# Kernel tuning notes

Measured on AMD Instinct MI355X. Metric: run time of the kernel, lower is better.

Reference implementation:

```python
import jax, jax.numpy as jnp
import numpy as np
from jax import lax

EPS = 1e-5  # torch BatchNorm default eps

# Binarization with straight-through estimator (hard-tanh gradient window),
# matching BinaryFunc in dizcza/MCMC_BinaryNet.
@jax.custom_vjp
def binarize(x):
    return jnp.sign(x)

def _bin_fwd(x):
    return jnp.sign(x), x

def _bin_bwd(res, g):
    return (g * (jnp.abs(res) <= 1.0).astype(g.dtype),)

binarize.defvjp(_bin_fwd, _bin_bwd)

def bn2d(x, gamma, beta):
    # training-mode BatchNorm2d: batch stats over (N,H,W), biased variance
    m = x.mean(axis=(0, 2, 3), keepdims=True)
    v = x.var(axis=(0, 2, 3), keepdims=True)
    xn = (x - m) * lax.rsqrt(v + EPS)
    return xn * gamma[None, :, None, None] + beta[None, :, None, None]

def bn1d(x, gamma, beta):
    m = x.mean(axis=0, keepdims=True)
    v = x.var(axis=0, keepdims=True)
    return (x - m) * lax.rsqrt(v + EPS) * gamma[None, :] + beta[None, :]

def bconv(x, w):
    # BinaryDecorator(Conv2d): sign(x) conv sign(W), padding=0, no bias
    return lax.conv_general_dilated(binarize(x), binarize(w), (1, 1), 'VALID',
                                    dimension_numbers=('NCHW', 'OIHW', 'NCHW'))

def maxpool2(x):
    return lax.reduce_window(x, -jnp.inf, lax.max, (1, 1, 2, 2), (1, 1, 2, 2), 'VALID')

def prelu(x, a):
    return jnp.where(x >= 0, x, a * x)


def setup_inputs() -> dict:
    key = jax.random.key(0)
    ks = iter(jax.random.split(key, 16))
    conv_channels = [3, 128, 256, 512]
    fc_sizes = [512 * 6 * 6, 1024, 10]
    d = {'x': jax.random.normal(next(ks), (128, 3, 64, 64), jnp.float32)}
    for i, (cin, cout) in enumerate(zip(conv_channels[:-1], conv_channels[1:])):
        d[f'cg{i}'] = jnp.ones((cin,), jnp.float32)          # BN2d gamma
        d[f'cb{i}'] = jnp.zeros((cin,), jnp.float32)         # BN2d beta
        d[f'cw{i}'] = jax.random.normal(next(ks), (cout, cin, 3, 3), jnp.float32) * 0.05
        d[f'cp{i}'] = jnp.full((1,), 0.25, jnp.float32)      # PReLU (num_parameters=1)
    for i, (fin, fout) in enumerate(zip(fc_sizes[:-1], fc_sizes[1:])):
        d[f'fg{i}'] = jnp.ones((fin,), jnp.float32)
        d[f'fb{i}'] = jnp.zeros((fin,), jnp.float32)
        d[f'fw{i}'] = jax.random.normal(next(ks), (fout, fin), jnp.float32) * 0.05
        d[f'fp{i}'] = jnp.full((1,), 0.25, jnp.float32)
    d['scale'] = jnp.full((1,), 1e-3, jnp.float32)           # ScaleLayer init
    return d


def reference(x, cg0, cb0, cw0, cp0, cg1, cb1, cw1, cp1, cg2, cb2, cw2, cp2,
              fg0, fb0, fw0, fp0, fg1, fb1, fw1, fp1, scale):
    for cg, cb, cw, cp in ((cg0, cb0, cw0, cp0), (cg1, cb1, cw1, cp1), (cg2, cb2, cw2, cp2)):
        x = bn2d(x, cg, cb)
        x = bconv(x, cw)
        x = maxpool2(x)
        x = prelu(x, cp)
    x = x.reshape(x.shape[0], -1)  # [B, 512*6*6]
    for fg, fb, fw, fp in ((fg0, fb0, fw0, fp0), (fg1, fb1, fw1, fp1)):
        x = bn1d(x, fg, fb)
        x = binarize(x) @ binarize(fw).T  # BinaryDecorator(Linear), no bias
        x = prelu(x, fp)
    return x * scale
```

## Files before the change

kernel.cpp:

```cpp
#include <hip/hip_runtime.h>
#include <cstdint>
#include <cstddef>

#define BN_EPS 1e-5


__global__ void zero_d(double* p, int n) {
  int i = blockIdx.x * blockDim.x + threadIdx.x;
  if (i < n) p[i] = 0.0;
}

__global__ void reduce_plane_p(const float* __restrict__ x, double* __restrict__ pp,
                               int C, int HW) {
  int c = blockIdx.x, n = blockIdx.y;
  const float* p = x + ((long)n * C + c) * HW;
  double s = 0.0, s2 = 0.0;
  for (int i = threadIdx.x; i < HW; i += blockDim.x) {
    double v = (double)p[i];
    s += v; s2 += v * v;
  }
  for (int o = 32; o > 0; o >>= 1) {
    s  += __shfl_down(s, o, 64);
    s2 += __shfl_down(s2, o, 64);
  }
  __shared__ double ls[4], ls2[4];
  int lane = threadIdx.x & 63, w = threadIdx.x >> 6;
  if (lane == 0) { ls[w] = s; ls2[w] = s2; }
  __syncthreads();
  if (threadIdx.x == 0) {
    double a = 0, b = 0;
    for (int i = 0; i < 4; i++) { a += ls[i]; b += ls2[i]; }
    long o = ((long)n * C + c) * 2;
    pp[o] = a; pp[o + 1] = b;
  }
}

__global__ void finalize_plane_par(const double* __restrict__ pp, double2* __restrict__ st,
                                   int C, int N, double cnt) {
  int c = blockIdx.x;
  double s = 0.0, s2 = 0.0;
  for (int n = threadIdx.x; n < N; n += blockDim.x) {
    long o = ((long)n * C + c) * 2;
    s  += pp[o];
    s2 += pp[o + 1];
  }
  for (int o = 32; o > 0; o >>= 1) {
    s  += __shfl_down(s, o, 64);
    s2 += __shfl_down(s2, o, 64);
  }
  __shared__ double ls[2], ls2[2];
  int lane = threadIdx.x & 63, w = threadIdx.x >> 6;
  if (lane == 0) { ls[w] = s; ls2[w] = s2; }
  __syncthreads();
  if (threadIdx.x == 0) {
    double a = ls[0] + ls[1], b = ls2[0] + ls2[1];
    double m = a / cnt;
    double v = b / cnt - m * m;
    st[c] = make_double2(m, 1.0 / sqrt(v + BN_EPS));
  }
}

__global__ void reduce_cl_p(const float* __restrict__ x, double* __restrict__ part,
                            int C, long rows) {
  int lane = threadIdx.x & 63, wv = threadIdx.x >> 6;
  int c = blockIdx.x * 64 + lane;
  double s = 0.0, s2 = 0.0;
  for (long r = (long)blockIdx.y * 4 + wv; r < rows; r += (long)gridDim.y * 4) {
    double v = (double)x[r * C + c];
    s += v; s2 += v * v;
  }
  __shared__ double ls[4][64], ls2[4][64];
  ls[wv][lane] = s; ls2[wv][lane] = s2;
  __syncthreads();
  if (threadIdx.x < 64) {
    double a = ls[0][lane] + ls[1][lane] + ls[2][lane] + ls[3][lane];
    double b = ls2[0][lane] + ls2[1][lane] + ls2[2][lane] + ls2[3][lane];
    long o = (long)blockIdx.y * 2 * C + 2 * c;
    part[o] = a; part[o + 1] = b;
  }
}

__global__ void finalize_parts_par(const double* __restrict__ part, double2* __restrict__ st,
                                   int C, int Y, double cnt) {
  int c = blockIdx.x;
  double s = 0.0, s2 = 0.0;
  for (int y = threadIdx.x; y < Y; y += blockDim.x) {
    long o = (long)y * 2 * C + 2 * c;
    s  += part[o];
    s2 += part[o + 1];
  }
  for (int o = 32; o > 0; o >>= 1) {
    s  += __shfl_down(s, o, 64);
    s2 += __shfl_down(s2, o, 64);
  }
  __shared__ double ls[4], ls2[4];
  int lane = threadIdx.x & 63, w = threadIdx.x >> 6;
  if (lane == 0) { ls[w] = s; ls2[w] = s2; }
  __syncthreads();
  if (threadIdx.x == 0) {
    double a = ls[0] + ls[1] + ls[2] + ls[3];
    double b = ls2[0] + ls2[1] + ls2[2] + ls2[3];
    double m = a / cnt;
    double v = b / cnt - m * m;
    st[c] = make_double2(m, 1.0 / sqrt(v + BN_EPS));
  }
}

__global__ void reduce_cols2(const float* __restrict__ x, double* __restrict__ sums,
                             int R, int F, int RS) {
  int f = blockIdx.x * blockDim.x + threadIdx.x;
  int r0 = blockIdx.y * RS, r1 = min(r0 + RS, R);
  double s = 0.0, s2 = 0.0;
  for (int r = r0; r < r1; r++) {
    double v = (double)x[(long)r * F + f];
    s += v; s2 += v * v;
  }
  atomicAdd(&sums[2 * f], s);
  atomicAdd(&sums[2 * f + 1], s2);
}

__global__ void finalize_stats(const double* __restrict__ sums, double2* __restrict__ st,
                               int C, double cnt) {
  int c = blockIdx.x * blockDim.x + threadIdx.x;
  if (c >= C) return;
  double m = sums[2 * c] / cnt;
  double v = sums[2 * c + 1] / cnt - m * m;
  st[c] = make_double2(m, 1.0 / sqrt(v + BN_EPS));
}


__global__ void pack_bits_c1(const float* __restrict__ x, const double2* __restrict__ st,
                             const float* __restrict__ g, const float* __restrict__ b,
                             uint64_t* __restrict__ rows, int nwid) {
  long base = ((long)blockIdx.x * 4 + (threadIdx.x >> 6)) * 8;
  int lane = threadIdx.x & 63;
  for (int j = 0; j < 8; j++) {
    long wid = base + j;
    if (wid >= nwid) return;
    int n = (int)(wid / 192), rem = (int)(wid % 192);
    int ci = rem >> 6, y = rem & 63;
    double2 s = st[ci];
    float xv = x[(((long)n * 3 + ci) * 64 + y) * 64 + lane];
    float xn = (float)(((double)xv - s.x) * s.y) * g[ci] + b[ci];
    uint64_t m = __ballot(xn > 0.f);
    if (lane == 0) rows[wid] = m;
  }
}

__global__ void pack_wc1(const float* __restrict__ w, uint32_t* __restrict__ wm) {
  int co = threadIdx.x;
  uint32_t m = 0;
  for (int j = 0; j < 27; j++) m |= (uint32_t)(w[co * 27 + j] > 0.f) << j;
  wm[co] = m;
}

__global__ void pack_cl(const float* __restrict__ acl, const double2* __restrict__ st,
                        const float* __restrict__ g, const float* __restrict__ b,
                        uint64_t* __restrict__ out, int C, long nwords, int lw) {
  long base = ((long)blockIdx.x * 4 + (threadIdx.x >> 6)) * 8;
  int lane = threadIdx.x & 63;
  for (int j = 0; j < 8; j++) {
    long wid = base + j;
    if (wid >= nwords) return;
    long row = wid >> lw;
    int w = (int)(wid & ((1 << lw) - 1));
    int c = w * 64 + lane;
    double2 s = st[c];
    float xv = acl[row * C + c];
    float xn = (float)(((double)xv - s.x) * s.y) * g[c] + b[c];
    uint64_t m = __ballot(xn > 0.f);
    if (lane == 0) out[wid] = m;
  }
}

__global__ void pack_wconv(const float* __restrict__ w, uint64_t* __restrict__ out,
                           int CO, int CI, int W) {
  int i = blockIdx.x * blockDim.x + threadIdx.x;
  int total = CO * 9 * W;
  if (i >= total) return;
  int wd = i % W;
  int t = i / W;
  int tap = t % 9, co = t / 9;
  uint64_t bits = 0;
  for (int k = 0; k < 64; k++) {
    int ci = wd * 64 + k;
    bits |= (uint64_t)(w[((long)co * CI + ci) * 9 + tap] > 0.f) << k;
  }
  out[i] = bits;
}

__global__ void pack_nz(const float* __restrict__ x, const double2* __restrict__ st,
                        const float* __restrict__ g, const float* __restrict__ b,
                        uint64_t* __restrict__ out, int R, int F) {
  int Wf = F >> 6;
  long base = ((long)blockIdx.x * 4 + (threadIdx.x >> 6)) * 8;
  int lane = threadIdx.x & 63;
  for (int j = 0; j < 8; j++) {
    long wid = base + j;
    if (wid >= (long)R * Wf) return;
    long r = wid / Wf;
    int w = (int)(wid % Wf);
    int f = w * 64 + lane;
    double2 s = st[f];
    double d = (double)x[r * F + f] - s.x;
    float xn = (float)(d * s.y) * g[f] + b[f];
    uint64_t sm = __ballot(xn > 0.f);
    uint64_t nm = __ballot(d != 0.0);
    if (lane == 0) { out[2 * wid] = sm; out[2 * wid + 1] = nm; }
  }
}

__global__ void pack_wfc2_t(const float* __restrict__ w, uint64_t* __restrict__ out,
                            int O, int F) {
  int Wf = F >> 6;
  long base = ((long)blockIdx.x * 4 + (threadIdx.x >> 6)) * 8;
  int lane = threadIdx.x & 63;
  for (int j = 0; j < 8; j++) {
    long wid = base + j;
    if (wid >= (long)O * Wf) return;
    long o = wid / Wf;
    int wd = (int)(wid % Wf);
    uint64_t m = __ballot(w[o * F + wd * 64 + lane] > 0.f);
    if (lane == 0) out[(long)wd * O + o] = m;
  }
}


__global__ __launch_bounds__(256) void conv1_pool3(const uint64_t* __restrict__ rows,
                                                   const uint32_t* __restrict__ wm,
                                                   const float* __restrict__ cp,
                                                   float* __restrict__ out) {
  __shared__ uint64_t rL[192];
  __shared__ uint32_t wL[128];
  __shared__ uint32_t mL[61 * 4];
  int n = blockIdx.y, chunk = blockIdx.x, t = threadIdx.x;
  if (t < 192) rL[t] = rows[n * 192 + t];
  if (t < 128) wL[t] = wm[t];
  __syncthreads();
  if (t < 244) {
    int pl = t >> 2, quad = t & 3;
    int pos = chunk * 61 + pl;
    if (pos < 961) {
      int py = pos / 31, px = pos - py * 31;
      int cy = 2 * py + (quad >> 1), cx = 2 * px + (quad & 1);
      uint32_t m = 0;
#pragma unroll
      for (int ci = 0; ci < 3; ci++)
#pragma unroll
        for (int ky = 0; ky < 3; ky++)
          m |= (uint32_t)((rL[ci * 64 + cy + ky] >> cx) & 7) << (ci * 9 + ky * 3);
      mL[pl * 4 + quad] = m;
    }
  }
  __syncthreads();
  int co = t & 127, slot = t >> 7;
  float alpha = cp[0];
  uint32_t w = wL[co];
  for (int i = slot; i < 61; i += 2) {
    int pos = chunk * 61 + i;
    if (pos >= 961) break;
    int p0 = __popc(mL[4 * i] ^ w);
    int p1 = __popc(mL[4 * i + 1] ^ w);
    int p2 = __popc(mL[4 * i + 2] ^ w);
    int p3 = __popc(mL[4 * i + 3] ^ w);
    int dot = 27 - 2 * min(min(p0, p1), min(p2, p3));
    float f = (float)dot;
    out[((long)n * 961 + pos) * 128 + co] = dot >= 0 ? f : alpha * f;
  }
}

template <int W, int IH, int PH, int CHUNK, bool CL>
__global__ __attribute__((amdgpu_flat_work_group_size(256, 256),
                          amdgpu_waves_per_eu(3, 4)))
void convp_carry(const uint64_t* __restrict__ in, const uint64_t* __restrict__ wt,
                 const float* __restrict__ cp, float* __restrict__ out, int CO) {
  __shared__ uint64_t sIn[10 * IH * W];
  int n = blockIdx.y;
  int cg = blockIdx.x / CHUNK, chunk = blockIdx.x % CHUNK;
  int t = threadIdx.x, lane = t & 63, slot = t >> 6;
  int r0 = chunk * 8;
  int nr = min(10, IH - r0);
  const uint64_t* src = in + ((long)n * IH + r0) * (IH * W);
  for (int i = t; i < nr * IH * W; i += 256) sIn[i] = src[i];
  int co = cg * 64 + lane;
  uint64_t wr[9 * W];
  const uint64_t* wg = wt + (long)co * (9 * W);
#pragma unroll
  for (int i = 0; i < 9 * W; i++) wr[i] = wg[i];
  __syncthreads();
  int py = chunk * 4 + slot;
  if (py >= PH) return;
  float alpha = cp[0];
  const int K = 9 * 64 * W;
  const uint64_t* base = &sIn[(2 * slot) * (IH * W)];
  uint64_t c[4][2 * W];
#pragma unroll
  for (int cy = 0; cy < 4; cy++) {
    const uint64_t* p = &base[(cy * IH) * W];
#pragma unroll
    for (int j = 0; j < 2 * W; j++) c[cy][j] = p[j];
  }
#pragma unroll
  for (int px = 0; px < PH; px++) {
    int a00 = 0, a01 = 0, a10 = 0, a11 = 0;
#pragma unroll
    for (int cy = 0; cy < 4; cy++) {
      uint64_t f[2 * W];
      const uint64_t* fp = &base[(cy * IH + 2 * px + 2) * W];
#pragma unroll
      for (int j = 0; j < 2 * W; j++) f[j] = fp[j];
#pragma unroll
      for (int col = 0; col < 4; col++) {
#pragma unroll
        for (int wd = 0; wd < W; wd++) {
          uint64_t v = (col < 2) ? c[cy][col * W + wd] : f[(col - 2) * W + wd];
#pragma unroll
          for (int dy = 0; dy < 2; dy++) {
            int ky = cy - dy;
            if (ky < 0 || ky > 2) continue;
#pragma unroll
            for (int dx = 0; dx < 2; dx++) {
              int kx = col - dx;
              if (kx < 0 || kx > 2) continue;
              int p = __popcll(v ^ wr[(ky * 3 + kx) * W + wd]);
              if (dy == 0) { if (dx == 0) a00 += p; else a01 += p; }
              else         { if (dx == 0) a10 += p; else a11 += p; }
            }
          }
        }
      }
#pragma unroll
      for (int j = 0; j < 2 * W; j++) c[cy][j] = f[j];
    }
    int dot = K - 2 * min(min(a00, a01), min(a10, a11));
    float f = (float)dot;
    long idx = CL ? (((long)n * PH * PH + py * PH + px) * CO + co)
                  : (((long)n * CO + co) * PH * PH + (py * PH + px));
    out[idx] = dot >= 0 ? f : alpha * f;
  }
}

#define TAP2(acc, P, wa, wb) acc += __popcll((P).x ^ (wa)) + __popcll((P).y ^ (wb));
#define ROWT(aL, aR, pA, pB, pC, pD, WX, WY, WZ)                \
  TAP2(aL, pA, WX.x, WX.y) TAP2(aL, pB, WY.x, WY.y)             \
  TAP2(aL, pC, WZ.x, WZ.y)                                      \
  TAP2(aR, pB, WX.x, WX.y) TAP2(aR, pC, WY.x, WY.y)             \
  TAP2(aR, pD, WZ.x, WZ.y)

__global__ __attribute__((amdgpu_flat_work_group_size(256, 256),
                          amdgpu_waves_per_eu(4, 6)))
void convs3(const uint64_t* __restrict__ in, const uint64_t* __restrict__ wt,
            const float* __restrict__ cp, float* __restrict__ out) {
  __shared__ uint64_t sIn[14 * 14 * 4];
  int n = blockIdx.y, cg = blockIdx.x;
  int t = threadIdx.x, lane = t & 63, slot = t >> 6;
  const uint64_t* src = in + (long)n * 784;
  for (int i = t; i < 784; i += 256) sIn[i] = src[i];
  int h = lane >> 5;
  int co = cg * 32 + (lane & 31);
  const uint64_t* wg = wt + co * 36 + 2 * h;
  ulonglong2 W0 = *(const ulonglong2*)(wg + 0);
  ulonglong2 W1 = *(const ulonglong2*)(wg + 4);
  ulonglong2 W2 = *(const ulonglong2*)(wg + 8);
  ulonglong2 W3 = *(const ulonglong2*)(wg + 12);
  ulonglong2 W4 = *(const ulonglong2*)(wg + 16);
  ulonglong2 W5 = *(const ulonglong2*)(wg + 20);
  ulonglong2 W6 = *(const ulonglong2*)(wg + 24);
  ulonglong2 W7 = *(const ulonglong2*)(wg + 28);
  ulonglong2 W8 = *(const ulonglong2*)(wg + 32);
  __syncthreads();
  float alpha = cp[0];
  float* outb = out + ((long)n * 512 + co) * 36;
#pragma unroll
  for (int k = 0; k < 9; k++) {
    int pos = slot + 4 * k;
    int py = pos / 6, px = pos - py * 6;
    const uint64_t* q = sIn + ((2 * py) * 14 + 2 * px) * 4 + 2 * h;
    int a00 = 0, a01 = 0, a10 = 0, a11 = 0;
    {
      ulonglong2 p0 = *(const ulonglong2*)(q + 0);
      ulonglong2 p1 = *(const ulonglong2*)(q + 4);
      ulonglong2 p2 = *(const ulonglong2*)(q + 8);
      ulonglong2 p3 = *(const ulonglong2*)(q + 12);
      ROWT(a00, a01, p0, p1, p2, p3, W0, W1, W2)
    }
    {
      const uint64_t* q1 = q + 56;
      ulonglong2 p0 = *(const ulonglong2*)(q1 + 0);
      ulonglong2 p1 = *(const ulonglong2*)(q1 + 4);
      ulonglong2 p2 = *(const ulonglong2*)(q1 + 8);
      ulonglong2 p3 = *(const ulonglong2*)(q1 + 12);
      ROWT(a00, a01, p0, p1, p2, p3, W3, W4, W5)
      ROWT(a10, a11, p0, p1, p2, p3, W0, W1, W2)
    }
    {
      const uint64_t* q2 = q + 112;
      ulonglong2 p0 = *(const ulonglong2*)(q2 + 0);
      ulonglong2 p1 = *(const ulonglong2*)(q2 + 4);
      ulonglong2 p2 = *(const ulonglong2*)(q2 + 8);
      ulonglong2 p3 = *(const ulonglong2*)(q2 + 12);
      ROWT(a00, a01, p0, p1, p2, p3, W6, W7, W8)
      ROWT(a10, a11, p0, p1, p2, p3, W3, W4, W5)
    }
    {
      const uint64_t* q3 = q + 168;
      ulonglong2 p0 = *(const ulonglong2*)(q3 + 0);
      ulonglong2 p1 = *(const ulonglong2*)(q3 + 4);
      ulonglong2 p2 = *(const ulonglong2*)(q3 + 8);
      ulonglong2 p3 = *(const ulonglong2*)(q3 + 12);
      ROWT(a10, a11, p0, p1, p2, p3, W6, W7, W8)
    }
    int t00 = a00 + __shfl_xor(a00, 32);
    int t01 = a01 + __shfl_xor(a01, 32);
    int t10 = a10 + __shfl_xor(a10, 32);
    int t11 = a11 + __shfl_xor(a11, 32);
    if (h == 0) {
      int dot = 2304 - 2 * min(min(t00, t01), min(t10, t11));
      float ff = (float)dot;
      outb[pos] = dot >= 0 ? ff : alpha * ff;
    }
  }
}


__global__ void fc_bin2(const uint64_t* __restrict__ xp, const uint64_t* __restrict__ wp_t,
                        const float* __restrict__ cp, float* __restrict__ out,
                        int O, int Wf) {
  __shared__ uint64_t xs[2][288], xz[2][288];
  int r0 = blockIdx.y * 2;
  for (int i = threadIdx.x; i < 2 * Wf; i += blockDim.x) {
    int rr = i / Wf, wd = i - rr * Wf;
    xs[rr][wd] = xp[(((long)(r0 + rr)) * Wf + wd) * 2];
    xz[rr][wd] = xp[(((long)(r0 + rr)) * Wf + wd) * 2 + 1];
  }
  __syncthreads();
  int o = blockIdx.x * blockDim.x + threadIdx.x;
  if (o >= O) return;
  int pc0 = 0, pc1 = 0, nz0 = 0, nz1 = 0;
  for (int wd = 0; wd < Wf; wd++) {
    uint64_t w = wp_t[(long)wd * O + o];
    uint64_t z0 = xz[0][wd], z1 = xz[1][wd];
    pc0 += __popcll((xs[0][wd] ^ w) & z0);
    pc1 += __popcll((xs[1][wd] ^ w) & z1);
    nz0 += __popcll(z0);
    nz1 += __popcll(z1);
  }
  float alpha = cp[0];
  int d0 = nz0 - 2 * pc0, d1 = nz1 - 2 * pc1;
  float f0 = (float)d0, f1 = (float)d1;
  out[(long)r0 * O + o] = d0 >= 0 ? f0 : alpha * f0;
  out[(long)(r0 + 1) * O + o] = d1 >= 0 ? f1 : alpha * f1;
}

__global__ void fc_bin_scale(const uint64_t* __restrict__ xp, const uint64_t* __restrict__ wp_t,
                             const float* __restrict__ cp, const float* __restrict__ scale,
                             float* __restrict__ out, int R, int O, int Wf) {
  int i = blockIdx.x * blockDim.x + threadIdx.x;
  if (i >= R * O) return;
  int o = i % O, r = i / O;
  int pc = 0, nzc = 0;
  for (int wd = 0; wd < Wf; wd++) {
    uint64_t nz = xp[((long)r * Wf + wd) * 2 + 1];
    pc += __popcll((xp[((long)r * Wf + wd) * 2] ^ wp_t[(long)wd * O + o]) & nz);
    nzc += __popcll(nz);
  }
  int dot = nzc - 2 * pc;
  float f = (float)dot;
  float alpha = cp[0];
  f = dot >= 0 ? f : alpha * f;
  out[i] = f * scale[0];
}


extern "C" void kernel_launch(void* const* d_in, const int* in_sizes, int n_in,
                              void* d_out, int out_size, void* d_ws, size_t ws_size,
                              hipStream_t stream) {
  const float* x   = (const float*)d_in[0];
  const float* cg0 = (const float*)d_in[1];
  const float* cb0 = (const float*)d_in[2];
  const float* cw0 = (const float*)d_in[3];
  const float* cp0 = (const float*)d_in[4];
  const float* cg1 = (const float*)d_in[5];
  const float* cb1 = (const float*)d_in[6];
  const float* cw1 = (const float*)d_in[7];
  const float* cp1 = (const float*)d_in[8];
  const float* cg2 = (const float*)d_in[9];
  const float* cb2 = (const float*)d_in[10];
  const float* cw2 = (const float*)d_in[11];
  const float* cp2 = (const float*)d_in[12];
  const float* fg0 = (const float*)d_in[13];
  const float* fb0 = (const float*)d_in[14];
  const float* fw0 = (const float*)d_in[15];
  const float* fp0 = (const float*)d_in[16];
  const float* fg1 = (const float*)d_in[17];
  const float* fb1 = (const float*)d_in[18];
  const float* fw1 = (const float*)d_in[19];
  const float* fp1 = (const float*)d_in[20];
  const float* scl = (const float*)d_in[21];

  char* ws = (char*)d_ws;
  size_t off = 0;
  auto alloc = [&](size_t bytes) {
    size_t r = off;
    off += (bytes + 255) & ~(size_t)255;
    return r;
  };
  const int C0_OFF = 0, C1_OFF = 16, C2_OFF = 160, C3_OFF = 448, C4_OFF = 18944;
  const int NCH = 19968;

  double*   sums  = (double*)(ws + alloc((size_t)NCH * 2 * sizeof(double)));
  double2*  stats = (double2*)(ws + alloc((size_t)NCH * sizeof(double2)));
  double*   parts = (double*)(ws + alloc(512L * 512 * sizeof(double)));
  double*   pplane= (double*)(ws + alloc(128L * 3 * 2 * sizeof(double)));
  uint64_t* rows0 = (uint64_t*)(ws + alloc(128L * 3 * 64 * 8));
  uint32_t* wm1   = (uint32_t*)(ws + alloc(128L * 4));
  float*    a1    = (float*)(ws + alloc(128L * 961 * 128 * 4));
  uint64_t* s1p   = (uint64_t*)(ws + alloc(128L * 961 * 2 * 8));
  uint64_t* w1p   = (uint64_t*)(ws + alloc(256L * 9 * 2 * 8));
  float*    a2    = (float*)(ws + alloc(128L * 196 * 256 * 4));
  uint64_t* s2p   = (uint64_t*)(ws + alloc(128L * 196 * 4 * 8));
  uint64_t* w2p   = (uint64_t*)(ws + alloc(512L * 9 * 4 * 8));
  float*    a3    = (float*)(ws + alloc(128L * 512 * 36 * 4));
  uint64_t* s3p   = (uint64_t*)(ws + alloc(128L * 288 * 2 * 8));
  uint64_t* w3p   = (uint64_t*)(ws + alloc(1024L * 288 * 8));
  float*    f1    = (float*)(ws + alloc(128L * 1024 * 4));
  uint64_t* s4p   = (uint64_t*)(ws + alloc(128L * 16 * 2 * 8));
  uint64_t* w4p   = (uint64_t*)(ws + alloc(10L * 16 * 8));

  const int B = 256;

  zero_d<<<dim3(153), B, 0, stream>>>(sums + 2 * C3_OFF, (NCH - C3_OFF) * 2);

  reduce_plane_p<<<dim3(3, 128), B, 0, stream>>>(x, pplane, 3, 4096);
  finalize_plane_par<<<dim3(3), 128, 0, stream>>>(pplane, stats + C0_OFF, 3, 128, 524288.0);
  pack_bits_c1<<<dim3(768), B, 0, stream>>>(x, stats + C0_OFF, cg0, cb0, rows0, 24576);
  pack_wc1<<<1, 128, 0, stream>>>(cw0, wm1);
  conv1_pool3<<<dim3(16, 128), B, 0, stream>>>(rows0, wm1, cp0, a1);

  reduce_cl_p<<<dim3(2, 512), B, 0, stream>>>(a1, parts, 128, 123008L);
  finalize_parts_par<<<dim3(128), B, 0, stream>>>(parts, stats + C1_OFF, 128, 512, 123008.0);
  pack_cl<<<dim3(7688), B, 0, stream>>>(a1, stats + C1_OFF, cg1, cb1, s1p, 128, 246016L, 1);
  pack_wconv<<<dim3(18), B, 0, stream>>>(cw1, w1p, 256, 128, 2);
  convp_carry<2, 31, 14, 4, true><<<dim3(16, 128), B, 0, stream>>>(s1p, w1p, cp1, a2, 256);

  reduce_cl_p<<<dim3(4, 256), B, 0, stream>>>(a2, parts, 256, 25088L);
  finalize_parts_par<<<dim3(256), B, 0, stream>>>(parts, stats + C2_OFF, 256, 256, 25088.0);
  pack_cl<<<dim3(3136), B, 0, stream>>>(a2, stats + C2_OFF, cg2, cb2, s2p, 256, 100352L, 2);
  pack_wconv<<<dim3(72), B, 0, stream>>>(cw2, w2p, 512, 256, 4);
  convs3<<<dim3(16, 128), B, 0, stream>>>(s2p, w2p, cp2, a3);

  reduce_cols2<<<dim3(72, 8), B, 0, stream>>>(a3, sums + 2 * C3_OFF, 128, 18432, 16);
  finalize_stats<<<dim3(72), B, 0, stream>>>(sums + 2 * C3_OFF, stats + C3_OFF, 18432, 128.0);
  pack_nz<<<dim3(1152), B, 0, stream>>>(a3, stats + C3_OFF, fg0, fb0, s3p, 128, 18432);
  pack_wfc2_t<<<dim3(9216), B, 0, stream>>>(fw0, w3p, 1024, 18432);
  fc_bin2<<<dim3(4, 64), B, 0, stream>>>(s3p, w3p, fp0, f1, 1024, 288);

  reduce_cols2<<<dim3(4, 8), B, 0, stream>>>(f1, sums + 2 * C4_OFF, 128, 1024, 16);
  finalize_stats<<<dim3(4), B, 0, stream>>>(sums + 2 * C4_OFF, stats + C4_OFF, 1024, 128.0);
  pack_nz<<<dim3(64), B, 0, stream>>>(f1, stats + C4_OFF, fg1, fb1, s4p, 128, 1024);
  pack_wfc2_t<<<dim3(5), B, 0, stream>>>(fw1, w4p, 10, 1024);
  fc_bin_scale<<<dim3(5), B, 0, stream>>>(s4p, w4p, fp1, scl, (float*)d_out, 128, 10, 16);
}
```

Before: 511.9 us.

## Store conv activations as int8/int16 and fuse BN statistics into conv epilogues

Conv outputs are now written as raw integer dot products (int8 for conv1, int16 for conv2/conv3), and PReLU is reapplied when they are read back, which cuts activation memory traffic by a factor of two to four. The conv1 and conv2 kernels also accumulate per-block partial sums and sums of squares for the next BatchNorm. This removes the separate reduce_cl_p passes over the activations, and new finalize kernels reduce those partials instead. The cost is extra per-thread double-precision accumulation and a shared-memory reduction in the conv epilogues.

```diff
diff --git a/kernel.cpp b/kernel.cpp
--- a/kernel.cpp
+++ b/kernel.cpp
@@ -60,34 +60,13 @@
   }
 }
 
-__global__ void reduce_cl_p(const float* __restrict__ x, double* __restrict__ part,
-                            int C, long rows) {
-  int lane = threadIdx.x & 63, wv = threadIdx.x >> 6;
-  int c = blockIdx.x * 64 + lane;
-  double s = 0.0, s2 = 0.0;
-  for (long r = (long)blockIdx.y * 4 + wv; r < rows; r += (long)gridDim.y * 4) {
-    double v = (double)x[r * C + c];
-    s += v; s2 += v * v;
-  }
-  __shared__ double ls[4][64], ls2[4][64];
-  ls[wv][lane] = s; ls2[wv][lane] = s2;
-  __syncthreads();
-  if (threadIdx.x < 64) {
-    double a = ls[0][lane] + ls[1][lane] + ls[2][lane] + ls[3][lane];
-    double b = ls2[0][lane] + ls2[1][lane] + ls2[2][lane] + ls2[3][lane];
-    long o = (long)blockIdx.y * 2 * C + 2 * c;
-    part[o] = a; part[o + 1] = b;
-  }
-}
-
-__global__ void finalize_parts_par(const double* __restrict__ part, double2* __restrict__ st,
-                                   int C, int Y, double cnt) {
+__global__ void finalize_pp1(const double2* __restrict__ pp, double2* __restrict__ st,
+                             int C, int Y, double cnt) {
   int c = blockIdx.x;
   double s = 0.0, s2 = 0.0;
   for (int y = threadIdx.x; y < Y; y += blockDim.x) {
-    long o = (long)y * 2 * C + 2 * c;
-    s  += part[o];
-    s2 += part[o + 1];
+    double2 p = pp[(long)y * C + c];
+    s += p.x; s2 += p.y;
   }
   for (int o = 32; o > 0; o >>= 1) {
     s  += __shfl_down(s, o, 64);
@@ -104,6 +83,49 @@
     double v = b / cnt - m * m;
     st[c] = make_double2(m, 1.0 / sqrt(v + BN_EPS));
   }
+}
+
+__global__ void finalize_pp2(const double2* __restrict__ pp, double2* __restrict__ st,
+                             double cnt) {
+  int c = blockIdx.x;
+  int cg = c >> 6, l = c & 63;
+  double s = 0.0, s2 = 0.0;
+  for (int y = threadIdx.x; y < 512; y += blockDim.x) {
+    int n = y >> 2, ch = y & 3;
+    double2 p = pp[(long)(n * 16 + cg * 4 + ch) * 64 + l];
+    s += p.x; s2 += p.y;
+  }
+  for (int o = 32; o > 0; o >>= 1) {
+    s  += __shfl_down(s, o, 64);
+    s2 += __shfl_down(s2, o, 64);
+  }
+  __shared__ double ls[4], ls2[4];
+  int lane = threadIdx.x & 63, w = threadIdx.x >> 6;
+  if (lane == 0) { ls[w] = s; ls2[w] = s2; }
+  __syncthreads();
+  if (threadIdx.x == 0) {
+    double a = ls[0] + ls[1] + ls[2] + ls[3];
+    double b = ls2[0] + ls2[1] + ls2[2] + ls2[3];
+    double m = a / cnt;
+    double v = b / cnt - m * m;
+    st[c] = make_double2(m, 1.0 / sqrt(v + BN_EPS));
+  }
+}
+
+__global__ void reduce_cols2_i16(const short* __restrict__ x, const float* __restrict__ cp,
+                                 double* __restrict__ sums, int R, int F, int RS) {
+  int f = blockIdx.x * blockDim.x + threadIdx.x;
+  int r0 = blockIdx.y * RS, r1 = min(r0 + RS, R);
+  float alpha = cp[0];
+  double s = 0.0, s2 = 0.0;
+  for (int r = r0; r < r1; r++) {
+    int xi = x[(long)r * F + f];
+    float pr = xi >= 0 ? (float)xi : alpha * (float)xi;
+    double v = (double)pr;
+    s += v; s2 += v * v;
+  }
+  atomicAdd(&sums[2 * f], s);
+  atomicAdd(&sums[2 * f + 1], s2);
 }
 
 __global__ void reduce_cols2(const float* __restrict__ x, double* __restrict__ sums,
@@ -154,11 +176,13 @@
   wm[co] = m;
 }
 
-__global__ void pack_cl(const float* __restrict__ acl, const double2* __restrict__ st,
-                        const float* __restrict__ g, const float* __restrict__ b,
-                        uint64_t* __restrict__ out, int C, long nwords, int lw) {
+__global__ void pack_cl_i8(const signed char* __restrict__ acl, const double2* __restrict__ st,
+                           const float* __restrict__ g, const float* __restrict__ b,
+                           const float* __restrict__ cp, uint64_t* __restrict__ out,
+                           int C, long nwords, int lw) {
   long base = ((long)blockIdx.x * 4 + (threadIdx.x >> 6)) * 8;
   int lane = threadIdx.x & 63;
+  float alpha = cp[0];
   for (int j = 0; j < 8; j++) {
     long wid = base + j;
     if (wid >= nwords) return;
@@ -166,8 +190,31 @@
     int w = (int)(wid & ((1 << lw) - 1));
     int c = w * 64 + lane;
     double2 s = st[c];
-    float xv = acl[row * C + c];
-    float xn = (float)(((double)xv - s.x) * s.y) * g[c] + b[c];
+    int xi = acl[row * C + c];
+    float pr = xi >= 0 ? (float)xi : alpha * (float)xi;
+    float xn = (float)(((double)pr - s.x) * s.y) * g[c] + b[c];
+    uint64_t m = __ballot(xn > 0.f);
+    if (lane == 0) out[wid] = m;
+  }
+}
+
+__global__ void pack_cl_i16(const short* __restrict__ acl, const double2* __restrict__ st,
+                            const float* __restrict__ g, const float* __restrict__ b,
+                            const float* __restrict__ cp, uint64_t* __restrict__ out,
+                            int C, long nwords, int lw) {
+  long base = ((long)blockIdx.x * 4 + (threadIdx.x >> 6)) * 8;
+  int lane = threadIdx.x & 63;
+  float alpha = cp[0];
+  for (int j = 0; j < 8; j++) {
+    long wid = base + j;
+    if (wid >= nwords) return;
+    long row = wid >> lw;
+    int w = (int)(wid & ((1 << lw) - 1));
+    int c = w * 64 + lane;
+    double2 s = st[c];
+    int xi = acl[row * C + c];
+    float pr = xi >= 0 ? (float)xi : alpha * (float)xi;
+    float xn = (float)(((double)pr - s.x) * s.y) * g[c] + b[c];
     uint64_t m = __ballot(xn > 0.f);
     if (lane == 0) out[wid] = m;
   }
@@ -187,6 +234,31 @@
     bits |= (uint64_t)(w[((long)co * CI + ci) * 9 + tap] > 0.f) << k;
   }
   out[i] = bits;
+}
+
+__global__ void pack_nz_i16(const short* __restrict__ x, const double2* __restrict__ st,
+                            const float* __restrict__ g, const float* __restrict__ b,
+                            const float* __restrict__ cp, uint64_t* __restrict__ out,
+                            int R, int F) {
+  int Wf = F >> 6;
+  long base = ((long)blockIdx.x * 4 + (threadIdx.x >> 6)) * 8;
+  int lane = threadIdx.x & 63;
+  float alpha = cp[0];
+  for (int j = 0; j < 8; j++) {
+    long wid = base + j;
+    if (wid >= (long)R * Wf) return;
+    long r = wid / Wf;
+    int w = (int)(wid % Wf);
+    int f = w * 64 + lane;
+    double2 s = st[f];
+    int xi = x[r * F + f];
+    float pr = xi >= 0 ? (float)xi : alpha * (float)xi;
+    double d = (double)pr - s.x;
+    float xn = (float)(d * s.y) * g[f] + b[f];
+    uint64_t sm = __ballot(xn > 0.f);
+    uint64_t nm = __ballot(d != 0.0);
+    if (lane == 0) { out[2 * wid] = sm; out[2 * wid + 1] = nm; }
+  }
 }
 
 __global__ void pack_nz(const float* __restrict__ x, const double2* __restrict__ st,
@@ -226,13 +298,15 @@
 }
 
 
-__global__ __launch_bounds__(256) void conv1_pool3(const uint64_t* __restrict__ rows,
-                                                   const uint32_t* __restrict__ wm,
-                                                   const float* __restrict__ cp,
-                                                   float* __restrict__ out) {
+__global__ __launch_bounds__(256) void conv1_pool3_i8(const uint64_t* __restrict__ rows,
+                                                      const uint32_t* __restrict__ wm,
+                                                      const float* __restrict__ cp,
+                                                      signed char* __restrict__ out,
+                                                      double2* __restrict__ pp) {
   __shared__ uint64_t rL[192];
   __shared__ uint32_t wL[128];
   __shared__ uint32_t mL[61 * 4];
+  __shared__ double2 sm[256];
   int n = blockIdx.y, chunk = blockIdx.x, t = threadIdx.x;
   if (t < 192) rL[t] = rows[n * 192 + t];
   if (t < 128) wL[t] = wm[t];
@@ -256,6 +330,7 @@
   int co = t & 127, slot = t >> 7;
   float alpha = cp[0];
   uint32_t w = wL[co];
+  double s = 0.0, s2 = 0.0;
   for (int i = slot; i < 61; i += 2) {
     int pos = chunk * 61 + i;
     if (pos >= 961) break;
@@ -264,17 +339,27 @@
     int p2 = __popc(mL[4 * i + 2] ^ w);
     int p3 = __popc(mL[4 * i + 3] ^ w);
     int dot = 27 - 2 * min(min(p0, p1), min(p2, p3));
-    float f = (float)dot;
-    out[((long)n * 961 + pos) * 128 + co] = dot >= 0 ? f : alpha * f;
-  }
-}
-
-template <int W, int IH, int PH, int CHUNK, bool CL>
+    out[((long)n * 961 + pos) * 128 + co] = (signed char)dot;
+    float pr = dot >= 0 ? (float)dot : alpha * (float)dot;
+    double v = (double)pr;
+    s += v; s2 += v * v;
+  }
+  sm[t] = make_double2(s, s2);
+  __syncthreads();
+  if (t < 128) {
+    double2 a = sm[t], b = sm[t + 128];
+    pp[((long)n * 16 + chunk) * 128 + t] = make_double2(a.x + b.x, a.y + b.y);
+  }
+}
+
+template <int W, int IH, int PH, int CHUNK>
 __global__ __attribute__((amdgpu_flat_work_group_size(256, 256),
                           amdgpu_waves_per_eu(3, 4)))
-void convp_carry(const uint64_t* __restrict__ in, const uint64_t* __restrict__ wt,
-                 const float* __restrict__ cp, float* __restrict__ out, int CO) {
+void convp_carry_i16(const uint64_t* __restrict__ in, const uint64_t* __restrict__ wt,
+                     const float* __restrict__ cp, short* __restrict__ out,
+                     double2* __restrict__ pp, int CO) {
   __shared__ uint64_t sIn[10 * IH * W];
+  __shared__ double2 sm[256];
   int n = blockIdx.y;
   int cg = blockIdx.x / CHUNK, chunk = blockIdx.x % CHUNK;
   int t = threadIdx.x, lane = t & 63, slot = t >> 6;
@@ -289,54 +374,63 @@
   for (int i = 0; i < 9 * W; i++) wr[i] = wg[i];
   __syncthreads();
   int py = chunk * 4 + slot;
-  if (py >= PH) return;
-  float alpha = cp[0];
-  const int K = 9 * 64 * W;
-  const uint64_t* base = &sIn[(2 * slot) * (IH * W)];
-  uint64_t c[4][2 * W];
-#pragma unroll
-  for (int cy = 0; cy < 4; cy++) {
-    const uint64_t* p = &base[(cy * IH) * W];
-#pragma unroll
-    for (int j = 0; j < 2 * W; j++) c[cy][j] = p[j];
-  }
-#pragma unroll
-  for (int px = 0; px < PH; px++) {
-    int a00 = 0, a01 = 0, a10 = 0, a11 = 0;
+  float alpha = cp[0];
+  double s = 0.0, s2 = 0.0;
+  if (py < PH) {
+    const int K = 9 * 64 * W;
+    const uint64_t* base = &sIn[(2 * slot) * (IH * W)];
+    uint64_t c[4][2 * W];
 #pragma unroll
     for (int cy = 0; cy < 4; cy++) {
-      uint64_t f[2 * W];
-      const uint64_t* fp = &base[(cy * IH + 2 * px + 2) * W];
-#pragma unroll
-      for (int j = 0; j < 2 * W; j++) f[j] = fp[j];
-#pragma unroll
-      for (int col = 0; col < 4; col++) {
-#pragma unroll
-        for (int wd = 0; wd < W; wd++) {
-          uint64_t v = (col < 2) ? c[cy][col * W + wd] : f[(col - 2) * W + wd];
-#pragma unroll
-          for (int dy = 0; dy < 2; dy++) {
-            int ky = cy - dy;
-            if (ky < 0 || ky > 2) continue;
-#pragma unroll
-            for (int dx = 0; dx < 2; dx++) {
-              int kx = col - dx;
-              if (kx < 0 || kx > 2) continue;
-              int p = __popcll(v ^ wr[(ky * 3 + kx) * W + wd]);
-              if (dy == 0) { if (dx == 0) a00 += p; else a01 += p; }
-              else         { if (dx == 0) a10 += p; else a11 += p; }
+      const uint64_t* p = &base[(cy * IH) * W];
+#pragma unroll
+      for (int j = 0; j < 2 * W; j++) c[cy][j] = p[j];
+    }
+#pragma unroll
+    for (int px = 0; px < PH; px++) {
+      int a00 = 0, a01 = 0, a10 = 0, a11 = 0;
+#pragma unroll
+      for (int cy = 0; cy < 4; cy++) {
+        uint64_t f[2 * W];
+        const uint64_t* fp = &base[(cy * IH + 2 * px + 2) * W];
+#pragma unroll
+        for (int j = 0; j < 2 * W; j++) f[j] = fp[j];
+#pragma unroll
+        for (int col = 0; col < 4; col++) {
+#pragma unroll
+          for (int wd = 0; wd < W; wd++) {
+            uint64_t v = (col < 2) ? c[cy][col * W + wd] : f[(col - 2) * W + wd];
+#pragma unroll
+            for (int dy = 0; dy < 2; dy++) {
+              int ky = cy - dy;
+              if (ky < 0 || ky > 2) continue;
+#pragma unroll
+              for (int dx = 0; dx < 2; dx++) {
+                int kx = col - dx;
+                if (kx < 0 || kx > 2) continue;
+                int p = __popcll(v ^ wr[(ky * 3 + kx) * W + wd]);
+                if (dy == 0) { if (dx == 0) a00 += p; else a01 += p; }
+                else         { if (dx == 0) a10 += p; else a11 += p; }
+              }
             }
           }
         }
+#pragma unroll
+        for (int j = 0; j < 2 * W; j++) c[cy][j] = f[j];
       }
-#pragma unroll
-      for (int j = 0; j < 2 * W; j++) c[cy][j] = f[j];
-    }
-    int dot = K - 2 * min(min(a00, a01), min(a10, a11));
-    float f = (float)dot;
-    long idx = CL ? (((long)n * PH * PH + py * PH + px) * CO + co)
-                  : (((long)n * CO + co) * PH * PH + (py * PH + px));
-    out[idx] = dot >= 0 ? f : alpha * f;
+      int dot = K - 2 * min(min(a00, a01), min(a10, a11));
+      out[((long)n * PH * PH + py * PH + px) * CO + co] = (short)dot;
+      float pr = dot >= 0 ? (float)dot : alpha * (float)dot;
+      double v = (double)pr;
+      s += v; s2 += v * v;
+    }
+  }
+  sm[t] = make_double2(s, s2);
+  __syncthreads();
+  if (t < 64) {
+    double2 a = sm[t], b = sm[64 + t], cc = sm[128 + t], d = sm[192 + t];
+    pp[((long)blockIdx.y * 16 + blockIdx.x) * 64 + t] =
+        make_double2(a.x + b.x + cc.x + d.x, a.y + b.y + cc.y + d.y);
   }
 }
 
@@ -349,8 +443,8 @@
 
 __global__ __attribute__((amdgpu_flat_work_group_size(256, 256),
                           amdgpu_waves_per_eu(4, 6)))
-void convs3(const uint64_t* __restrict__ in, const uint64_t* __restrict__ wt,
-            const float* __restrict__ cp, float* __restrict__ out) {
+void convs3_i16(const uint64_t* __restrict__ in, const uint64_t* __restrict__ wt,
+                short* __restrict__ out) {
   __shared__ uint64_t sIn[14 * 14 * 4];
   int n = blockIdx.y, cg = blockIdx.x;
   int t = threadIdx.x, lane = t & 63, slot = t >> 6;
@@ -369,8 +463,7 @@
   ulonglong2 W7 = *(const ulonglong2*)(wg + 28);
   ulonglong2 W8 = *(const ulonglong2*)(wg + 32);
   __syncthreads();
-  float alpha = cp[0];
-  float* outb = out + ((long)n * 512 + co) * 36;
+  short* outb = out + ((long)n * 512 + co) * 36;
 #pragma unroll
   for (int k = 0; k < 9; k++) {
     int pos = slot + 4 * k;
@@ -416,8 +509,7 @@
     int t11 = a11 + __shfl_xor(a11, 32);
     if (h == 0) {
       int dot = 2304 - 2 * min(min(t00, t01), min(t10, t11));
-      float ff = (float)dot;
-      outb[pos] = dot >= 0 ? ff : alpha * ff;
+      outb[pos] = (short)dot;
     }
   }
 }
@@ -510,17 +602,18 @@
 
   double*   sums  = (double*)(ws + alloc((size_t)NCH * 2 * sizeof(double)));
   double2*  stats = (double2*)(ws + alloc((size_t)NCH * sizeof(double2)));
-  double*   parts = (double*)(ws + alloc(512L * 512 * sizeof(double)));
   double*   pplane= (double*)(ws + alloc(128L * 3 * 2 * sizeof(double)));
+  double2*  pp1   = (double2*)(ws + alloc(2048L * 128 * sizeof(double2)));
+  double2*  pp2   = (double2*)(ws + alloc(2048L * 64 * sizeof(double2)));
   uint64_t* rows0 = (uint64_t*)(ws + alloc(128L * 3 * 64 * 8));
   uint32_t* wm1   = (uint32_t*)(ws + alloc(128L * 4));
-  float*    a1    = (float*)(ws + alloc(128L * 961 * 128 * 4));
+  signed char* a1 = (signed char*)(ws + alloc(128L * 961 * 128));
   uint64_t* s1p   = (uint64_t*)(ws + alloc(128L * 961 * 2 * 8));
   uint64_t* w1p   = (uint64_t*)(ws + alloc(256L * 9 * 2 * 8));
-  float*    a2    = (float*)(ws + alloc(128L * 196 * 256 * 4));
+  short*    a2    = (short*)(ws + alloc(128L * 196 * 256 * 2));
   uint64_t* s2p   = (uint64_t*)(ws + alloc(128L * 196 * 4 * 8));
   uint64_t* w2p   = (uint64_t*)(ws + alloc(512L * 9 * 4 * 8));
-  float*    a3    = (float*)(ws + alloc(128L * 512 * 36 * 4));
+  short*    a3    = (short*)(ws + alloc(128L * 512 * 36 * 2));
   uint64_t* s3p   = (uint64_t*)(ws + alloc(128L * 288 * 2 * 8));
   uint64_t* w3p   = (uint64_t*)(ws + alloc(1024L * 288 * 8));
   float*    f1    = (float*)(ws + alloc(128L * 1024 * 4));
@@ -535,23 +628,21 @@
   finalize_plane_par<<<dim3(3), 128, 0, stream>>>(pplane, stats + C0_OFF, 3, 128, 524288.0);
   pack_bits_c1<<<dim3(768), B, 0, stream>>>(x, stats + C0_OFF, cg0, cb0, rows0, 24576);
   pack_wc1<<<1, 128, 0, stream>>>(cw0, wm1);
-  conv1_pool3<<<dim3(16, 128), B, 0, stream>>>(rows0, wm1, cp0, a1);
-
-  reduce_cl_p<<<dim3(2, 512), B, 0, stream>>>(a1, parts, 128, 123008L);
-  finalize_parts_par<<<dim3(128), B, 0, stream>>>(parts, stats + C1_OFF, 128, 512, 123008.0);
-  pack_cl<<<dim3(7688), B, 0, stream>>>(a1, stats + C1_OFF, cg1, cb1, s1p, 128, 246016L, 1);
+  conv1_pool3_i8<<<dim3(16, 128), B, 0, stream>>>(rows0, wm1, cp0, a1, pp1);
+
+  finalize_pp1<<<dim3(128), B, 0, stream>>>(pp1, stats + C1_OFF, 128, 2048, 123008.0);
+  pack_cl_i8<<<dim3(7688), B, 0, stream>>>(a1, stats + C1_OFF, cg1, cb1, cp0, s1p, 128, 246016L, 1);
   pack_wconv<<<dim3(18), B, 0, stream>>>(cw1, w1p, 256, 128, 2);
-  convp_carry<2, 31, 14, 4, true><<<dim3(16, 128), B, 0, stream>>>(s1p, w1p, cp1, a2, 256);
-
-  reduce_cl_p<<<dim3(4, 256), B, 0, stream>>>(a2, parts, 256, 25088L);
-  finalize_parts_par<<<dim3(256), B, 0, stream>>>(parts, stats + C2_OFF, 256, 256, 25088.0);
-  pack_cl<<<dim3(3136), B, 0, stream>>>(a2, stats + C2_OFF, cg2, cb2, s2p, 256, 100352L, 2);
+  convp_carry_i16<2, 31, 14, 4><<<dim3(16, 128), B, 0, stream>>>(s1p, w1p, cp1, a2, pp2, 256);
+
+  finalize_pp2<<<dim3(256), B, 0, stream>>>(pp2, stats + C2_OFF, 25088.0);
+  pack_cl_i16<<<dim3(3136), B, 0, stream>>>(a2, stats + C2_OFF, cg2, cb2, cp1, s2p, 256, 100352L, 2);
   pack_wconv<<<dim3(72), B, 0, stream>>>(cw2, w2p, 512, 256, 4);
-  convs3<<<dim3(16, 128), B, 0, stream>>>(s2p, w2p, cp2, a3);
-
-  reduce_cols2<<<dim3(72, 8), B, 0, stream>>>(a3, sums + 2 * C3_OFF, 128, 18432, 16);
+  convs3_i16<<<dim3(16, 128), B, 0, stream>>>(s2p, w2p, a3);
+
+  reduce_cols2_i16<<<dim3(72, 8), B, 0, stream>>>(a3, cp2, sums + 2 * C3_OFF, 128, 18432, 16);
   finalize_stats<<<dim3(72), B, 0, stream>>>(sums + 2 * C3_OFF, stats + C3_OFF, 18432, 128.0);
-  pack_nz<<<dim3(1152), B, 0, stream>>>(a3, stats + C3_OFF, fg0, fb0, s3p, 128, 18432);
+  pack_nz_i16<<<dim3(1152), B, 0, stream>>>(a3, stats + C3_OFF, fg0, fb0, cp2, s3p, 128, 18432);
   pack_wfc2_t<<<dim3(9216), B, 0, stream>>>(fw0, w3p, 1024, 18432);
   fc_bin2<<<dim3(4, 64), B, 0, stream>>>(s3p, w3p, fp0, f1, 1024, 288);
 
```

Result: faster. 494.7 us (-3.3%).
